# Kernel tuning notes

Hardware: AMD Instinct MI355X
Metric: run time of the kernel (lower is better)

Reference implementation:

```python
import jax, jax.numpy as jnp
import numpy as np

D_MODEL = 1024
N_HEADS = 16
HEAD_DIM = D_MODEL // N_HEADS
WINDOW = 256


def setup_inputs() -> dict:
    key = jax.random.key(0)
    kx, kq, ko = jax.random.split(key, 3)
    B, T = 4, 2048
    x = jax.random.normal(kx, (B, T, D_MODEL), dtype=jnp.float32)
    s = 1.0 / np.sqrt(D_MODEL)
    w_qkv = jax.random.normal(kq, (D_MODEL, 3 * D_MODEL), dtype=jnp.float32) * s
    w_out = jax.random.normal(ko, (D_MODEL, D_MODEL), dtype=jnp.float32) * s
    return {"x": x, "w_qkv": w_qkv, "w_out": w_out}


def reference(x, w_qkv, w_out):
    B, T, C = x.shape
    qkv = (x @ w_qkv).reshape(B, T, 3, N_HEADS, HEAD_DIM)
    q, k, v = qkv[:, :, 0], qkv[:, :, 1], qkv[:, :, 2]  # [B,T,H,D]
    # sliding-window causal mask: position i attends to j in (i-W, i]
    i = jnp.arange(T)[:, None]
    j = jnp.arange(T)[None, :]
    allowed = (j <= i) & (j > i - WINDOW)
    mask = jnp.where(allowed, 0.0, -jnp.inf).astype(x.dtype)  # [T,T]
    scale = 1.0 / np.sqrt(HEAD_DIM)
    scores = jnp.einsum('bqhd,bkhd->bhqk', q, k) * scale + mask
    attn = jax.nn.softmax(scores, axis=-1)
    out = jnp.einsum('bhqk,bkhd->bqhd', attn, v).reshape(B, T, C)
    return out @ w_out
```

## Files before the change

kernel.cpp:

```cpp
#include <hip/hip_runtime.h>

typedef unsigned short u16;
typedef __attribute__((ext_vector_type(8))) short bh8;
typedef __attribute__((ext_vector_type(4))) float f4;
typedef __attribute__((ext_vector_type(4))) unsigned short us4;

#define T_SEQ 2048
#define NHEADS 16
#define DHEAD 64
#define WIN 256

__device__ __forceinline__ float bf2f(u16 u) {
  union { unsigned int i; float f; } v; v.i = ((unsigned int)u) << 16; return v.f;
}
__device__ __forceinline__ u16 f2bf(float f) {
  unsigned int u = __float_as_uint(f);
  u = u + 0x7fffu + ((u >> 16) & 1u);
  return (u16)(u >> 16);
}
__device__ __forceinline__ void async16(const void* g, void* l) {
  void* gv = const_cast<void*>(g);
  __builtin_amdgcn_global_load_lds(
      (__attribute__((address_space(1))) void*)gv,
      (__attribute__((address_space(3))) void*)l, 16, 0, 0);
}

__device__ __forceinline__ int is_f32_probe(const void* x) {
  const float* xf = (const float*)x;
  const int lane = threadIdx.x & 63;
  int bad = 0;
  #pragma unroll
  for (int u = 0; u < 4; ++u) {
    const float v = xf[lane * 4 + u];
    const float a = fabsf(v);
    bad |= (!(a < 64.f)) || (!(v == 0.f || a > 1e-30f));
  }
  return __any(bad) ? 0 : 1;
}

__global__ __launch_bounds__(256) void prep(
    const void* __restrict__ x, const void* __restrict__ w_qkv,
    const void* __restrict__ w_out, u16* __restrict__ xbf,
    u16* __restrict__ wqkvT, u16* __restrict__ woutT, int have_x)
{
  const int bid = blockIdx.x;
  const int tid = threadIdx.x;
  const int isf = is_f32_probe(x);

  if (bid < 4096) {
    if (!have_x) return;
    const size_t e = ((size_t)bid * 256 + tid) * 8;
    if (isf) {
      const float* f = (const float*)x;
      us4 o0, o1;
      #pragma unroll
      for (int u = 0; u < 4; ++u) { o0[u] = f2bf(f[e + u]); o1[u] = f2bf(f[e + 4 + u]); }
      *(us4*)&xbf[e] = o0; *(us4*)&xbf[e + 4] = o1;
    } else {
      *(us4*)&xbf[e]     = *(const us4*)&((const u16*)x)[e];
      *(us4*)&xbf[e + 4] = *(const us4*)&((const u16*)x)[e + 4];
    }
  } else {
    __shared__ alignas(16) u16 tile[32][33];
    const void* in; u16* out; int C, bx, by;
    if (bid < 4096 + 3072) { const int t = bid - 4096; in = w_qkv; out = wqkvT; C = 3072; bx = t % 96; by = t / 96; }
    else                   { const int t = bid - 7168; in = w_out; out = woutT; C = 1024; bx = t % 32; by = t / 32; }
    const int R = 1024;
    const int tx = tid & 31, ty = tid >> 5;
    const int xg = bx * 32 + tx;
    const int y0 = by * 32;
    #pragma unroll
    for (int i = ty; i < 32; i += 8) {
      u16 v;
      if (isf) v = f2bf(((const float*)in)[(size_t)(y0 + i) * C + xg]);
      else     v = ((const u16*)in)[(size_t)(y0 + i) * C + xg];
      tile[i][tx] = v;
    }
    __syncthreads();
    const int ox  = y0 + tx;
    const int oy0 = bx * 32;
    #pragma unroll
    for (int i = ty; i < 32; i += 8)
      out[(size_t)(oy0 + i) * R + ox] = tile[tx][i];
  }
}

template<bool ADYN, bool CDYN>
__global__ __launch_bounds__(256, 4) void gemm_bt(
    const void* __restrict__ A, const u16* __restrict__ Bt,
    void* __restrict__ C, int N, int K, int lda, int ldc,
    const void* __restrict__ xprobe)
{
  __shared__ alignas(16) u16 As[128 * 64];
  __shared__ alignas(16) u16 Bs[128 * 64];

  const int isf  = (ADYN || CDYN) ? is_f32_probe(xprobe) : 0;
  const int tid  = threadIdx.x;
  const int lane = tid & 63;
  const int w    = tid >> 6;
  const int wm   = (w >> 1) * 64;
  const int wn   = (w & 1) * 64;
  const int quad = lane >> 4;
  const int l16  = lane & 15;
  const int row0 = blockIdx.y * 128;
  const int col0 = blockIdx.x * 128;

  f4 acc[4][4] = {};

  size_t aoff[4]; const u16* bsrc[4]; int lofs[4];
  #pragma unroll
  for (int s = 0; s < 4; ++s) {
    const int r  = s * 32 + (tid >> 3);
    const int gc = (tid & 7) ^ (r & 7);
    aoff[s] = (size_t)(row0 + r) * lda + gc * 8;
    bsrc[s] = Bt + (size_t)(col0 + r) * K + gc * 8;
    lofs[s] = s * 4096 + tid * 16;
  }

  const bool af32 = ADYN && isf;

  for (int k0 = 0; k0 < K; k0 += 64) {
    if (af32) {
      const float* Af = (const float*)A;
      bh8 a[4];
      #pragma unroll
      for (int s = 0; s < 4; ++s) {
        f4 u0 = *(const f4*)(Af + aoff[s] + k0);
        f4 u1 = *(const f4*)(Af + aoff[s] + k0 + 4);
        #pragma unroll
        for (int u = 0; u < 4; ++u) { a[s][u] = (short)f2bf(u0[u]); a[s][u + 4] = (short)f2bf(u1[u]); }
      }
      __syncthreads();
      #pragma unroll
      for (int s = 0; s < 4; ++s) {
        *(bh8*)((char*)As + lofs[s]) = a[s];
        async16(bsrc[s] + k0, (char*)Bs + lofs[s]);
      }
    } else {
      const u16* A16 = (const u16*)A;
      __syncthreads();
      #pragma unroll
      for (int s = 0; s < 4; ++s) {
        async16(A16 + aoff[s] + k0, (char*)As + lofs[s]);
        async16(bsrc[s] + k0,       (char*)Bs + lofs[s]);
      }
    }
    __builtin_amdgcn_s_waitcnt(0);
    __syncthreads();

    #pragma unroll
    for (int ks = 0; ks < 2; ++ks) {
      bh8 af[4], bf[4];
      #pragma unroll
      for (int i = 0; i < 4; ++i) {
        const int row = wm + i * 16 + l16;
        const int lc  = (ks * 4 + quad) ^ (row & 7);
        af[i] = *(const bh8*)(As + row * 64 + lc * 8);
      }
      #pragma unroll
      for (int j = 0; j < 4; ++j) {
        const int row = wn + j * 16 + l16;
        const int lc  = (ks * 4 + quad) ^ (row & 7);
        bf[j] = *(const bh8*)(Bs + row * 64 + lc * 8);
      }
      #pragma unroll
      for (int i = 0; i < 4; ++i)
        #pragma unroll
        for (int j = 0; j < 4; ++j)
          acc[i][j] = __builtin_amdgcn_mfma_f32_16x16x32_bf16(af[i], bf[j], acc[i][j], 0, 0, 0);
    }
  }

  const bool cf32 = CDYN && isf;
  #pragma unroll
  for (int i = 0; i < 4; ++i) {
    #pragma unroll
    for (int j = 0; j < 4; ++j) {
      const int rb = row0 + wm + i * 16 + quad * 4;
      const int cc = col0 + wn + j * 16 + l16;
      #pragma unroll
      for (int r = 0; r < 4; ++r) {
        if (cf32) ((float*)C)[(size_t)(rb + r) * ldc + cc] = acc[i][j][r];
        else      ((u16*)C)[(size_t)(rb + r) * ldc + cc]   = f2bf(acc[i][j][r]);
      }
    }
  }
}

__global__ __launch_bounds__(256) void attn_mfma(const u16* __restrict__ qkv,
                                                 u16* __restrict__ att, int ldo)
{
  __shared__ alignas(16) u16 Kt[64 * 72];
  __shared__ alignas(16) u16 Vt[64 * 72];
  __shared__ alignas(16) u16 Ps[64 * 72];

  const int tid  = threadIdx.x;
  const int lane = tid & 63;
  const int w    = tid >> 6;
  const int quad = lane >> 4;
  const int l16  = lane & 15;
  const int qb = blockIdx.x, h = blockIdx.y, b = blockIdx.z;
  const int qs = qb * 64;

  const u16* base = qkv + (size_t)b * T_SEQ * 3072 + h * 64;

  const size_t qrowg = (size_t)(qs + w * 16 + l16) * 3072;
  bh8 qa0 = *(const bh8*)&base[qrowg + quad * 8];
  bh8 qa1 = *(const bh8*)&base[qrowg + 32 + quad * 8];

  f4 Oc[4] = {};
  float mst[4] = {-1e30f, -1e30f, -1e30f, -1e30f};
  float lst[4] = {0.f, 0.f, 0.f, 0.f};

  const int tmin = (qb >= 4) ? 0 : (4 - qb);
  const int c8  = (tid & 7) * 8;
  const int r0s = tid >> 3;

  for (int t = tmin; t < 5; ++t) {
    const int kt0 = qs - 256 + t * 64;
    __syncthreads();

    #pragma unroll
    for (int r = r0s; r < 64; r += 32) {
      *(bh8*)&Kt[r * 72 + c8] =
          *(const bh8*)&base[(size_t)(kt0 + r) * 3072 + 1024 + c8];
      bh8 v = *(const bh8*)&base[(size_t)(kt0 + r) * 3072 + 2048 + c8];
      const int kc = r >> 3, ki = r & 7;
      #pragma unroll
      for (int u = 0; u < 8; ++u) {
        const int d = c8 + u;
        Vt[d * 72 + ((kc ^ (d >> 3)) << 3) + ki] = (u16)v[u];
      }
    }
    __syncthreads();

    f4 S[4];
    #pragma unroll
    for (int kb = 0; kb < 4; ++kb) {
      const int krow = (kb * 16 + l16) * 72;
      bh8 kf0 = *(const bh8*)&Kt[krow + quad * 8];
      bh8 kf1 = *(const bh8*)&Kt[krow + 32 + quad * 8];
      f4 s = {};
      s = __builtin_amdgcn_mfma_f32_16x16x32_bf16(qa0, kf0, s, 0, 0, 0);
      s = __builtin_amdgcn_mfma_f32_16x16x32_bf16(qa1, kf1, s, 0, 0, 0);
      S[kb] = s;
    }

    const int iq0 = qs + w * 16 + quad * 4;
    float tmax[4] = {-1e30f, -1e30f, -1e30f, -1e30f};
    #pragma unroll
    for (int kb = 0; kb < 4; ++kb) {
      const int j = kt0 + kb * 16 + l16;
      #pragma unroll
      for (int rr = 0; rr < 4; ++rr) {
        const int i = iq0 + rr;
        float s = S[kb][rr] * 0.125f;
        const bool ok = (j <= i) && (j > i - WIN);
        s = ok ? s : -1e30f;
        S[kb][rr] = s;
        tmax[rr] = fmaxf(tmax[rr], s);
      }
    }
    #pragma unroll
    for (int off = 1; off < 16; off <<= 1)
      #pragma unroll
      for (int rr = 0; rr < 4; ++rr)
        tmax[rr] = fmaxf(tmax[rr], __shfl_xor(tmax[rr], off));

    float alpha[4], rsum[4];
    #pragma unroll
    for (int rr = 0; rr < 4; ++rr) {
      const float mnew = fmaxf(mst[rr], tmax[rr]);
      alpha[rr] = __expf(mst[rr] - mnew);
      mst[rr] = mnew;
      rsum[rr] = 0.f;
    }

    const int swq = quad >> 1;
    #pragma unroll
    for (int kb = 0; kb < 4; ++kb) {
      const int kc = kb * 2 + (l16 >> 3);
      const int ki = l16 & 7;
      #pragma unroll
      for (int rr = 0; rr < 4; ++rr) {
        const float sv = S[kb][rr];
        const float p = (sv > -0.5e30f) ? __expf(sv - mst[rr]) : 0.f;
        rsum[rr] += p;
        const int q = w * 16 + quad * 4 + rr;
        Ps[q * 72 + ((kc ^ swq) << 3) + ki] = f2bf(p);
      }
    }
    #pragma unroll
    for (int off = 1; off < 16; off <<= 1)
      #pragma unroll
      for (int rr = 0; rr < 4; ++rr)
        rsum[rr] += __shfl_xor(rsum[rr], off);
    #pragma unroll
    for (int rr = 0; rr < 4; ++rr)
      lst[rr] = lst[rr] * alpha[rr] + rsum[rr];

    #pragma unroll
    for (int db = 0; db < 4; ++db)
      #pragma unroll
      for (int rr = 0; rr < 4; ++rr)
        Oc[db][rr] *= alpha[rr];

    {
      const int q = w * 16 + l16;
      const int sw = (q >> 3) & 1;
      bh8 pa0 = *(const bh8*)&Ps[q * 72 + (((0 + quad) ^ sw) << 3)];
      bh8 pa1 = *(const bh8*)&Ps[q * 72 + (((4 + quad) ^ sw) << 3)];
      #pragma unroll
      for (int db = 0; db < 4; ++db) {
        const int d = db * 16 + l16;
        const int dsw = d >> 3;
        bh8 vb0 = *(const bh8*)&Vt[d * 72 + (((0 + quad) ^ dsw) << 3)];
        bh8 vb1 = *(const bh8*)&Vt[d * 72 + (((4 + quad) ^ dsw) << 3)];
        Oc[db] = __builtin_amdgcn_mfma_f32_16x16x32_bf16(pa0, vb0, Oc[db], 0, 0, 0);
        Oc[db] = __builtin_amdgcn_mfma_f32_16x16x32_bf16(pa1, vb1, Oc[db], 0, 0, 0);
      }
    }
  }

  u16* obase = att + (size_t)b * T_SEQ * ldo + h * 64;
  #pragma unroll
  for (int rr = 0; rr < 4; ++rr) {
    const int i = qs + w * 16 + quad * 4 + rr;
    const float inv = 1.f / lst[rr];
    #pragma unroll
    for (int db = 0; db < 4; ++db)
      obase[(size_t)i * ldo + db * 16 + l16] = f2bf(Oc[db][rr] * inv);
  }
}

extern "C" void kernel_launch(void* const* d_in, const int* in_sizes, int n_in,
                              void* d_out, int out_size, void* d_ws, size_t ws_size,
                              hipStream_t stream) {
  const void* x     = d_in[0];
  const void* w_qkv = d_in[1];
  const void* w_out = d_in[2];

  const size_t SZ_QKV = (size_t)8192 * 3072 * 2;
  const size_t SZ_XBF = (size_t)8192 * 1024 * 2;
  const size_t SZ_WQ  = (size_t)3072 * 1024 * 2;
  const size_t SZ_WO  = (size_t)1024 * 1024 * 2;
  const size_t SZ_ATT = (size_t)8192 * 1024 * 2;

  char* p = (char*)d_ws;
  u16* qkv   = (u16*)p; p += SZ_QKV;
  u16* wqkvT = (u16*)p; p += SZ_WQ;
  u16* woutT = (u16*)p; p += SZ_WO;
  u16* xbf   = (u16*)p; p += SZ_XBF;
  u16* attb  = (u16*)p;
  const size_t need_x   = SZ_QKV + SZ_WQ + SZ_WO + SZ_XBF;
  const bool have_x   = ws_size >= need_x;
  const bool have_att = ws_size >= need_x + SZ_ATT;

  prep<<<dim3(8192), 256, 0, stream>>>(x, w_qkv, w_out, xbf, wqkvT, woutT,
                                       have_x ? 1 : 0);

  if (have_x) {
    gemm_bt<false, false><<<dim3(24, 64), 256, 0, stream>>>(
        xbf, wqkvT, qkv, 3072, 1024, 1024, 3072, x);
  } else {
    gemm_bt<true, false><<<dim3(24, 64), 256, 0, stream>>>(
        x, wqkvT, qkv, 3072, 1024, 1024, 3072, x);
  }

  u16* attp  = have_att ? attb : qkv;
  const int ldo = have_att ? 1024 : 3072;
  attn_mfma<<<dim3(32, NHEADS, 4), 256, 0, stream>>>(qkv, attp, ldo);

  gemm_bt<false, true><<<dim3(8, 64), 256, 0, stream>>>(
      attp, woutT, d_out, 1024, 1024, ldo, 1024, x);
}
```

Baseline: 225.0 us.

## Add 8-wave triple-buffered GEMM with interleaved async loads and MFMA priority

Adds a new GEMM kernel that uses 512 threads and 256x128 tiles. It keeps a three-stage LDS ring filled by async global-to-LDS loads, and splits each K step into four phases that interleave LDS reads, prefetches, barriers and setprio-raised MFMA blocks. Both the QKV projection and the output projection now use it. The goal is to hide global load latency and get more MFMA throughput than the old double-buffered 256-thread GEMM. In exchange it uses much more LDS and adds more barriers, which may limit occupancy, and the output projection now launches only 256 blocks.

```diff
diff --git a/kernel.cpp b/kernel.cpp
--- a/kernel.cpp
+++ b/kernel.cpp
@@ -9,6 +9,10 @@
 #define NHEADS 16
 #define DHEAD 64
 #define WIN 256
+
+#define MF(a, b, c) __builtin_amdgcn_mfma_f32_16x16x32_bf16((a), (b), (c), 0, 0, 0)
+#define BARX() asm volatile("s_barrier" ::: "memory")
+#define VMCNT(n) asm volatile("s_waitcnt vmcnt(" #n ")" ::: "memory")
 
 __device__ __forceinline__ float bf2f(u16 u) {
   union { unsigned int i; float f; } v; v.i = ((unsigned int)u) << 16; return v.f;
@@ -167,8 +171,151 @@
       for (int i = 0; i < 4; ++i)
         #pragma unroll
         for (int j = 0; j < 4; ++j)
-          acc[i][j] = __builtin_amdgcn_mfma_f32_16x16x32_bf16(af[i], bf[j], acc[i][j], 0, 0, 0);
-    }
+          acc[i][j] = MF(af[i], bf[j], acc[i][j]);
+    }
+  }
+
+  const bool cf32 = CDYN && isf;
+  #pragma unroll
+  for (int i = 0; i < 4; ++i) {
+    #pragma unroll
+    for (int j = 0; j < 4; ++j) {
+      const int rb = row0 + wm + i * 16 + quad * 4;
+      const int cc = col0 + wn + j * 16 + l16;
+      #pragma unroll
+      for (int r = 0; r < 4; ++r) {
+        if (cf32) ((float*)C)[(size_t)(rb + r) * ldc + cc] = acc[i][j][r];
+        else      ((u16*)C)[(size_t)(rb + r) * ldc + cc]   = f2bf(acc[i][j][r]);
+      }
+    }
+  }
+}
+
+template<bool CDYN>
+__global__ __launch_bounds__(512, 2) void gemm8(
+    const u16* __restrict__ A, const u16* __restrict__ Bt, void* __restrict__ C,
+    int K, int lda, int ldc, const void* __restrict__ xprobe)
+{
+  __shared__ alignas(16) u16 As[3 * 256 * 64];
+  __shared__ alignas(16) u16 Bs[3 * 128 * 64];
+
+  const int isf  = CDYN ? is_f32_probe(xprobe) : 0;
+  const int tid  = threadIdx.x;
+  const int lane = tid & 63;
+  const int w    = tid >> 6;
+  const int wm   = (w >> 1) * 64;
+  const int wn   = (w & 1) * 64;
+  const int quad = lane >> 4;
+  const int l16  = lane & 15;
+  const int row0 = blockIdx.y * 256;
+  const int col0 = blockIdx.x * 128;
+
+  f4 acc[4][4] = {};
+
+  const int rs = tid >> 3;
+  const int cs = tid & 7;
+  const u16* apt[4]; const u16* bpt[2]; int aofs[4], bofs[2];
+  #pragma unroll
+  for (int s = 0; s < 4; ++s) {
+    const int r = s * 64 + rs;
+    apt[s]  = A + (size_t)(row0 + r) * lda + (cs ^ (r & 7)) * 8;
+    aofs[s] = s * 8192 + tid * 16;
+  }
+  #pragma unroll
+  for (int s = 0; s < 2; ++s) {
+    const int r = s * 64 + rs;
+    bpt[s]  = Bt + (size_t)(col0 + r) * K + (cs ^ (r & 7)) * 8;
+    bofs[s] = s * 8192 + tid * 16;
+  }
+
+  const int NK = K >> 6;
+
+  const int sw = l16 & 7;
+  const int c0 = ((quad    ) ^ sw) * 8;
+  const int c1 = ((quad + 4) ^ sw) * 8;
+  const int ra0 = (wm      + l16) * 64, ra1 = (wm + 16 + l16) * 64,
+            ra2 = (wm + 32 + l16) * 64, ra3 = (wm + 48 + l16) * 64;
+  const int rb0 = (wn      + l16) * 64, rb1 = (wn + 16 + l16) * 64,
+            rb2 = (wn + 32 + l16) * 64, rb3 = (wn + 48 + l16) * 64;
+
+  #pragma unroll
+  for (int s = 0; s < 4; ++s) async16(apt[s], (char*)As + aofs[s]);
+  #pragma unroll
+  for (int s = 0; s < 2; ++s) async16(bpt[s], (char*)Bs + bofs[s]);
+  if (NK > 1) {
+    #pragma unroll
+    for (int s = 0; s < 4; ++s) async16(apt[s] + 64, (char*)As + 32768 + aofs[s]);
+    #pragma unroll
+    for (int s = 0; s < 2; ++s) async16(bpt[s] + 64, (char*)Bs + 16384 + bofs[s]);
+    VMCNT(6);
+  } else {
+    VMCNT(0);
+  }
+  BARX();
+
+  int cb = 0, sb = 2;
+  for (int kt = 0; kt < NK; ++kt) {
+    const u16* Ab = As + cb * 16384;
+    const u16* Bb = Bs + cb * 8192;
+    char* Asb = (char*)As + sb * 32768;
+    char* Bsb = (char*)Bs + sb * 16384;
+    const bool st = (kt + 2) < NK;
+    const int k2 = (kt + 2) * 64;
+
+    bh8 a00 = *(const bh8*)(Ab + ra0 + c0), a01 = *(const bh8*)(Ab + ra0 + c1);
+    bh8 a10 = *(const bh8*)(Ab + ra1 + c0), a11 = *(const bh8*)(Ab + ra1 + c1);
+    bh8 b00 = *(const bh8*)(Bb + rb0 + c0), b01 = *(const bh8*)(Bb + rb0 + c1);
+    bh8 b10 = *(const bh8*)(Bb + rb1 + c0), b11 = *(const bh8*)(Bb + rb1 + c1);
+    if (st) { async16(apt[0] + k2, Asb + aofs[0]);
+              async16(apt[1] + k2, Asb + aofs[1]); }
+    BARX();
+    __builtin_amdgcn_s_setprio(1);
+    acc[0][0] = MF(a01, b01, MF(a00, b00, acc[0][0]));
+    acc[0][1] = MF(a01, b11, MF(a00, b10, acc[0][1]));
+    acc[1][0] = MF(a11, b01, MF(a10, b00, acc[1][0]));
+    acc[1][1] = MF(a11, b11, MF(a10, b10, acc[1][1]));
+    __builtin_amdgcn_s_setprio(0);
+    BARX();
+
+    bh8 a20 = *(const bh8*)(Ab + ra2 + c0), a21 = *(const bh8*)(Ab + ra2 + c1);
+    bh8 a30 = *(const bh8*)(Ab + ra3 + c0), a31 = *(const bh8*)(Ab + ra3 + c1);
+    if (st) { async16(apt[2] + k2, Asb + aofs[2]);
+              async16(apt[3] + k2, Asb + aofs[3]); }
+    BARX();
+    __builtin_amdgcn_s_setprio(1);
+    acc[2][0] = MF(a21, b01, MF(a20, b00, acc[2][0]));
+    acc[2][1] = MF(a21, b11, MF(a20, b10, acc[2][1]));
+    acc[3][0] = MF(a31, b01, MF(a30, b00, acc[3][0]));
+    acc[3][1] = MF(a31, b11, MF(a30, b10, acc[3][1]));
+    __builtin_amdgcn_s_setprio(0);
+    BARX();
+
+    bh8 b20 = *(const bh8*)(Bb + rb2 + c0), b21 = *(const bh8*)(Bb + rb2 + c1);
+    bh8 b30 = *(const bh8*)(Bb + rb3 + c0), b31 = *(const bh8*)(Bb + rb3 + c1);
+    if (st) async16(bpt[0] + k2, Bsb + bofs[0]);
+    BARX();
+    __builtin_amdgcn_s_setprio(1);
+    acc[0][2] = MF(a01, b21, MF(a00, b20, acc[0][2]));
+    acc[0][3] = MF(a01, b31, MF(a00, b30, acc[0][3]));
+    acc[1][2] = MF(a11, b21, MF(a10, b20, acc[1][2]));
+    acc[1][3] = MF(a11, b31, MF(a10, b30, acc[1][3]));
+    __builtin_amdgcn_s_setprio(0);
+    BARX();
+
+    if (st) async16(bpt[1] + k2, Bsb + bofs[1]);
+    BARX();
+    __builtin_amdgcn_s_setprio(1);
+    acc[2][2] = MF(a21, b21, MF(a20, b20, acc[2][2]));
+    acc[2][3] = MF(a21, b31, MF(a20, b30, acc[2][3]));
+    acc[3][2] = MF(a31, b21, MF(a30, b20, acc[3][2]));
+    acc[3][3] = MF(a31, b31, MF(a30, b30, acc[3][3]));
+    __builtin_amdgcn_s_setprio(0);
+    if (st) VMCNT(6);
+    else    VMCNT(0);
+    BARX();
+
+    cb = (cb == 2) ? 0 : cb + 1;
+    sb = (sb == 2) ? 0 : sb + 1;
   }
 
   const bool cf32 = CDYN && isf;
@@ -360,8 +507,8 @@
                                        have_x ? 1 : 0);
 
   if (have_x) {
-    gemm_bt<false, false><<<dim3(24, 64), 256, 0, stream>>>(
-        xbf, wqkvT, qkv, 3072, 1024, 1024, 3072, x);
+    gemm8<false><<<dim3(24, 32), 512, 0, stream>>>(
+        xbf, wqkvT, qkv, 1024, 1024, 3072, x);
   } else {
     gemm_bt<true, false><<<dim3(24, 64), 256, 0, stream>>>(
         x, wqkvT, qkv, 3072, 1024, 1024, 3072, x);
@@ -371,6 +518,6 @@
   const int ldo = have_att ? 1024 : 3072;
   attn_mfma<<<dim3(32, NHEADS, 4), 256, 0, stream>>>(qkv, attp, ldo);
 
-  gemm_bt<false, true><<<dim3(8, 64), 256, 0, stream>>>(
-      attp, woutT, d_out, 1024, 1024, ldo, 1024, x);
-}
+  gemm8<true><<<dim3(8, 32), 512, 0, stream>>>(
+      attp, woutT, d_out, 1024, ldo, 1024, x);
+}
```

Result: slower. 238.7 us (+6.1%).

## Skip masked QK tiles, prescale Q, and use lazy softmax rescaling

Applied to the files above, without the earlier changes.

Folds the 1/sqrt(d) scale into the Q fragments once, removing the per-score multiply. It skips QK MFMAs for key blocks that are fully masked on the diagonal and left-edge tiles and applies the per-element mask only on those tiles. Online-softmax rescaling of O and l now happens only when some row's max grows by more than 8, a wave-uniform branch. The risks are one extra bf16 rounding of Q from prescaling and relying on exp(-1e30 - m) underflowing to zero for masked entries.

```diff
diff --git a/kernel.cpp b/kernel.cpp
--- a/kernel.cpp
+++ b/kernel.cpp
@@ -207,6 +207,11 @@
   const size_t qrowg = (size_t)(qs + w * 16 + l16) * 3072;
   bh8 qa0 = *(const bh8*)&base[qrowg + quad * 8];
   bh8 qa1 = *(const bh8*)&base[qrowg + 32 + quad * 8];
+  #pragma unroll
+  for (int u = 0; u < 8; ++u) {
+    qa0[u] = (short)f2bf(bf2f((u16)qa0[u]) * 0.125f);
+    qa1[u] = (short)f2bf(bf2f((u16)qa1[u]) * 0.125f);
+  }
 
   f4 Oc[4] = {};
   float mst[4] = {-1e30f, -1e30f, -1e30f, -1e30f};
@@ -218,6 +223,10 @@
 
   for (int t = tmin; t < 5; ++t) {
     const int kt0 = qs - 256 + t * 64;
+    const bool diag  = (t == 4);
+    const bool ledge = (t == 0);
+    const int kb_lo = ledge ? w : 0;
+    const int kb_hi = diag  ? w : 3;
     __syncthreads();
 
     #pragma unroll
@@ -237,45 +246,60 @@
     f4 S[4];
     #pragma unroll
     for (int kb = 0; kb < 4; ++kb) {
-      const int krow = (kb * 16 + l16) * 72;
-      bh8 kf0 = *(const bh8*)&Kt[krow + quad * 8];
-      bh8 kf1 = *(const bh8*)&Kt[krow + 32 + quad * 8];
-      f4 s = {};
-      s = __builtin_amdgcn_mfma_f32_16x16x32_bf16(qa0, kf0, s, 0, 0, 0);
-      s = __builtin_amdgcn_mfma_f32_16x16x32_bf16(qa1, kf1, s, 0, 0, 0);
-      S[kb] = s;
-    }
-
-    const int iq0 = qs + w * 16 + quad * 4;
+      if (kb < kb_lo || kb > kb_hi) {
+        S[kb][0] = S[kb][1] = S[kb][2] = S[kb][3] = -1e30f;
+      } else {
+        const int krow = (kb * 16 + l16) * 72;
+        bh8 kf0 = *(const bh8*)&Kt[krow + quad * 8];
+        bh8 kf1 = *(const bh8*)&Kt[krow + 32 + quad * 8];
+        f4 s = {};
+        s = __builtin_amdgcn_mfma_f32_16x16x32_bf16(qa0, kf0, s, 0, 0, 0);
+        s = __builtin_amdgcn_mfma_f32_16x16x32_bf16(qa1, kf1, s, 0, 0, 0);
+        S[kb] = s;
+      }
+    }
+
+    if (diag || ledge) {
+      #pragma unroll
+      for (int kb = 0; kb < 4; ++kb) {
+        if (kb == w) {
+          #pragma unroll
+          for (int rr = 0; rr < 4; ++rr) {
+            const int ii = quad * 4 + rr;
+            const bool ok = diag ? (l16 <= ii) : (l16 > ii);
+            if (!ok) S[kb][rr] = -1e30f;
+          }
+        }
+      }
+    }
+
     float tmax[4] = {-1e30f, -1e30f, -1e30f, -1e30f};
     #pragma unroll
-    for (int kb = 0; kb < 4; ++kb) {
-      const int j = kt0 + kb * 16 + l16;
-      #pragma unroll
-      for (int rr = 0; rr < 4; ++rr) {
-        const int i = iq0 + rr;
-        float s = S[kb][rr] * 0.125f;
-        const bool ok = (j <= i) && (j > i - WIN);
-        s = ok ? s : -1e30f;
-        S[kb][rr] = s;
-        tmax[rr] = fmaxf(tmax[rr], s);
-      }
-    }
+    for (int kb = 0; kb < 4; ++kb)
+      #pragma unroll
+      for (int rr = 0; rr < 4; ++rr)
+        tmax[rr] = fmaxf(tmax[rr], S[kb][rr]);
     #pragma unroll
     for (int off = 1; off < 16; off <<= 1)
       #pragma unroll
       for (int rr = 0; rr < 4; ++rr)
         tmax[rr] = fmaxf(tmax[rr], __shfl_xor(tmax[rr], off));
 
-    float alpha[4], rsum[4];
-    #pragma unroll
-    for (int rr = 0; rr < 4; ++rr) {
-      const float mnew = fmaxf(mst[rr], tmax[rr]);
-      alpha[rr] = __expf(mst[rr] - mnew);
-      mst[rr] = mnew;
-      rsum[rr] = 0.f;
-    }
-
+    const bool grew = (tmax[0] > mst[0] + 8.f) || (tmax[1] > mst[1] + 8.f) ||
+                      (tmax[2] > mst[2] + 8.f) || (tmax[3] > mst[3] + 8.f);
+    if (__any(grew)) {
+      #pragma unroll
+      for (int rr = 0; rr < 4; ++rr) {
+        const float mnew = fmaxf(mst[rr], tmax[rr]);
+        const float al = __expf(mst[rr] - mnew);
+        mst[rr] = mnew;
+        lst[rr] *= al;
+        #pragma unroll
+        for (int db = 0; db < 4; ++db) Oc[db][rr] *= al;
+      }
+    }
+
+    float rsum[4] = {0.f, 0.f, 0.f, 0.f};
     const int swq = quad >> 1;
     #pragma unroll
     for (int kb = 0; kb < 4; ++kb) {
@@ -283,8 +307,7 @@
       const int ki = l16 & 7;
       #pragma unroll
       for (int rr = 0; rr < 4; ++rr) {
-        const float sv = S[kb][rr];
-        const float p = (sv > -0.5e30f) ? __expf(sv - mst[rr]) : 0.f;
+        const float p = __expf(S[kb][rr] - mst[rr]);
         rsum[rr] += p;
         const int q = w * 16 + quad * 4 + rr;
         Ps[q * 72 + ((kc ^ swq) << 3) + ki] = f2bf(p);
@@ -297,13 +320,7 @@
         rsum[rr] += __shfl_xor(rsum[rr], off);
     #pragma unroll
     for (int rr = 0; rr < 4; ++rr)
-      lst[rr] = lst[rr] * alpha[rr] + rsum[rr];
-
-    #pragma unroll
-    for (int db = 0; db < 4; ++db)
-      #pragma unroll
-      for (int rr = 0; rr < 4; ++rr)
-        Oc[db][rr] *= alpha[rr];
+      lst[rr] += rsum[rr];
 
     {
       const int q = w * 16 + l16;
```

After: 226.6 us. Within noise of the previous version (+0.7%).
